# Kernel tuning notes

Measured on AMD Instinct MI355X. Metric: run time of the kernel, lower is better.

The kernel has to match this reference:

```python
import jax, jax.numpy as jnp
import numpy as np

N_NODES = 50000
N_EDGES = 1000000
HIDDEN = 64
NUM_GRAPHS = 512
EPS = 1e-5


def _instance_norm(x, seg, num_graphs):
    # per-graph, per-channel normalization (PyG InstanceNorm, affine=False)
    ones = jnp.ones((x.shape[0], 1), x.dtype)
    cnt = jnp.clip(jax.ops.segment_sum(ones, seg, num_segments=num_graphs), 1.0)
    mean = jax.ops.segment_sum(x, seg, num_segments=num_graphs) / cnt
    xc = x - mean[seg]
    var = jax.ops.segment_sum(xc * xc, seg, num_segments=num_graphs) / cnt
    return xc * jax.lax.rsqrt(var + EPS)[seg]


def setup_inputs() -> dict:
    key = jax.random.key(0)
    ks = jax.random.split(key, 10)
    emb = jax.random.normal(ks[0], (N_NODES, HIDDEN), jnp.float32)
    edge_index = jax.random.randint(ks[1], (2, N_EDGES), 0, N_NODES, jnp.int64 if jax.config.read('jax_enable_x64') else jnp.int32)
    batch = jnp.sort(jax.random.randint(ks[2], (N_NODES,), 0, NUM_GRAPHS))
    h = HIDDEN
    # channels = [2h, 4h, h, 1]
    W1 = jax.random.normal(ks[3], (2 * h, 4 * h), jnp.float32) * 0.05
    b1 = jnp.zeros((4 * h,), jnp.float32)
    W2 = jax.random.normal(ks[4], (4 * h, h), jnp.float32) * 0.05
    b2 = jnp.zeros((h,), jnp.float32)
    W3 = jax.random.normal(ks[5], (h, 1), jnp.float32) * 0.05
    b3 = jnp.zeros((1,), jnp.float32)
    return {"emb": emb, "W1": W1, "b1": b1, "W2": W2, "b2": b2,
            "W3": W3, "b3": b3, "edge_index": edge_index, "batch": batch}


def reference(emb, W1, b1, W2, b2, W3, b3, edge_index, batch):
    col, row = edge_index[0], edge_index[1]
    f12 = jnp.concatenate([emb[col], emb[row]], axis=-1)  # [E, 2h]
    seg = batch[col]  # per-edge graph id
    x = f12 @ W1 + b1                                      # [E, 4h]
    x = jax.nn.relu(_instance_norm(x, seg, NUM_GRAPHS))
    x = x @ W2 + b2                                        # [E, h]
    x = jax.nn.relu(_instance_norm(x, seg, NUM_GRAPHS))
    return x @ W3 + b3                                     # [E, 1]
```

## Files before the change

### kernel.cpp

```cpp
#include <hip/hip_runtime.h>
#include <hip/hip_bf16.h>

#define EDGES 1000000
#define NNODES 50000
#define NG 512
#define NTILES 15625
#define NCOLB 50176

typedef __attribute__((ext_vector_type(8))) short bf16x8;
typedef __attribute__((ext_vector_type(4))) float f32x4;

__device__ __forceinline__ unsigned short f2bf(float f){
  unsigned u = __float_as_uint(f);
  u += 0x7fffu + ((u >> 16) & 1u);
  return (unsigned short)(u >> 16);
}
__device__ __forceinline__ float bf2f(unsigned short h){
  return __uint_as_float(((unsigned)h) << 16);
}
__device__ __forceinline__ unsigned pk2bf(float x, float y){
  __hip_bfloat162 h = __float22bfloat162_rn(make_float2(x, y));
  union { __hip_bfloat162 h; unsigned u; } cv; cv.h = h;
  return cv.u;
}
__device__ __forceinline__ int xcd_swizzle(int bid, int nb){
  int nb8 = nb & ~7;
  if (bid >= nb8) return bid;
  int per = nb8 >> 3;
  return (bid & 7) * per + (bid >> 3);
}

__global__ void prep_all(const float* __restrict__ emb, const float* __restrict__ W1,
                         const float* __restrict__ W2,
                         unsigned short* __restrict__ emb_bf,
                         unsigned short* __restrict__ w1tn, unsigned short* __restrict__ w2t){
  int i = blockIdx.x * 256 + threadIdx.x;
  if (i < NNODES * 64){
    emb_bf[i] = f2bf(emb[i]);
  } else {
    int j = i - NNODES * 64;
    if (j < 32768){
      int jj = j >> 6, k = j & 63;
      float v = (jj < 256) ? W1[k * 256 + jj] : W1[(k + 64) * 256 + (jj - 256)];
      w1tn[j] = f2bf(v);
    } else {
      int jj = j - 32768;
      if (jj < 16384){
        int n = jj >> 8, k = jj & 255;
        w2t[jj] = f2bf(W2[k * 64 + n]);
      }
    }
  }
}

__global__ void hists(const int* __restrict__ ei, const int* __restrict__ batch,
                      unsigned* __restrict__ hist, unsigned* __restrict__ chist){
  __shared__ unsigned h[NG];
  int t = threadIdx.x;
  h[t] = 0; h[t + 256] = 0;
  __syncthreads();
  for (int i = 0; i < 4; i++){
    int e = blockIdx.x * 1024 + i * 256 + t;
    if (e < EDGES){
      int cn = ei[e];
      atomicAdd(&chist[cn], 1u);
      atomicAdd(&h[batch[cn]], 1u);
    }
  }
  __syncthreads();
  atomicAdd(&hist[t], h[t]);
  atomicAdd(&hist[t + 256], h[t + 256]);
}

__global__ void col_scan1(const unsigned* __restrict__ chist, unsigned* __restrict__ cpre,
                          unsigned* __restrict__ bsum){
  __shared__ unsigned s[256];
  int t = threadIdx.x;
  int i = blockIdx.x * 256 + t;
  unsigned v = (i < NNODES) ? chist[i] : 0u;
  s[t] = v;
  __syncthreads();
  for (int o = 1; o < 256; o <<= 1){
    unsigned u = (t >= o) ? s[t - o] : 0u;
    __syncthreads();
    s[t] += u;
    __syncthreads();
  }
  cpre[i] = s[t] - v;
  if (t == 255) bsum[blockIdx.x] = s[255];
}

__global__ void col_scan2(unsigned* __restrict__ bsum){
  __shared__ unsigned s[256];
  int t = threadIdx.x;
  unsigned v = (t < 196) ? bsum[t] : 0u;
  s[t] = v;
  __syncthreads();
  for (int o = 1; o < 256; o <<= 1){
    unsigned u = (t >= o) ? s[t - o] : 0u;
    __syncthreads();
    s[t] += u;
    __syncthreads();
  }
  if (t < 196) bsum[t] = s[t] - v;
}

__global__ void col_scan3(unsigned* __restrict__ cpre, const unsigned* __restrict__ bsum){
  int i = blockIdx.x * 256 + threadIdx.x;
  cpre[i] += bsum[blockIdx.x];
}

__global__ void col_scatter(const int* __restrict__ ei, const int* __restrict__ batch,
                            unsigned* __restrict__ cpre, int4* __restrict__ emeta){
  for (int i = 0; i < 4; i++){
    int e = blockIdx.x * 1024 + i * 256 + threadIdx.x;
    if (e < EDGES){
      int cn = ei[e];
      int pos = (int)atomicAdd(&cpre[cn], 1u);
      emeta[pos] = make_int4(cn, ei[EDGES + e], batch[cn], e);
    }
  }
}

__global__ __launch_bounds__(256) void node_gemm(
    const unsigned short* __restrict__ emb_bf, const unsigned short* __restrict__ w1tn,
    unsigned short* __restrict__ P)
{
  __shared__ unsigned short As[64 * 72];
  int t = threadIdx.x;
  int n0 = blockIdx.x * 64;
  {
    int nl = t >> 2, part = t & 3;
    int node = n0 + nl; if (node >= NNODES) node = 0;
    const int4* src = (const int4*)(emb_bf + node * 64 + part * 16);
    int4* dst = (int4*)(As + nl * 72 + part * 16);
    dst[0] = src[0]; dst[1] = src[1];
  }
  __syncthreads();
  int w = t >> 6, lane = t & 63, q = lane >> 4, c = lane & 15;
  f32x4 acc[4][8];
  for (int a = 0; a < 4; a++) for (int b = 0; b < 8; b++) for (int r = 0; r < 4; r++) acc[a][b][r] = 0.f;
  for (int k0 = 0; k0 < 64; k0 += 32){
    bf16x8 af[4];
    for (int tt = 0; tt < 4; tt++) af[tt] = *(const bf16x8*)(As + (tt * 16 + c) * 72 + k0 + q * 8);
    for (int n4 = 0; n4 < 8; n4++){
      bf16x8 bw = *(const bf16x8*)(w1tn + (w * 128 + n4 * 16 + c) * 64 + k0 + q * 8);
      for (int tt = 0; tt < 4; tt++)
        acc[tt][n4] = __builtin_amdgcn_mfma_f32_16x16x32_bf16(af[tt], bw, acc[tt][n4], 0, 0, 0);
    }
  }
  for (int tt = 0; tt < 4; tt++){
    for (int r = 0; r < 4; r++){
      int node = n0 + tt * 16 + q * 4 + r;
      if (node < NNODES){
        unsigned short* dst = P + (size_t)node * 512 + w * 128 + c;
        for (int n4 = 0; n4 < 8; n4++) dst[n4 * 16] = f2bf(acc[tt][n4][r]);
      }
    }
  }
}

__global__ __launch_bounds__(256) void k1_gather(
    const unsigned short* __restrict__ P, const int4* __restrict__ emeta,
    float* __restrict__ sum1, float* __restrict__ sqs1)
{
  int lane = threadIdx.x & 63;
  int bid = xcd_swizzle(blockIdx.x, gridDim.x);
  int wid = (bid * 256 + threadIdx.x) >> 6;
  if (wid >= NTILES) return;
  int p0 = wid * 64;
  int4 me = emeta[p0 + lane];
  int c4 = lane * 4;
  int s0 = __builtin_amdgcn_readlane(me.z, 0);
  bool uni = (__ballot(me.z == s0) == ~0ull);
  float sm0 = 0.f, sm1 = 0.f, sm2 = 0.f, sm3 = 0.f;
  float q0 = 0.f, q1 = 0.f, q2 = 0.f, q3 = 0.f;
  if (uni){
    int cprev = __builtin_amdgcn_readlane(me.x, 0);
    ushort4 a = *(const ushort4*)(P + (size_t)cprev * 512 + c4);
    ushort4 cur[4];
    #pragma unroll
    for (int j = 0; j < 4; j++){
      int re = __builtin_amdgcn_readlane(me.y, j);
      cur[j] = *(const ushort4*)(P + (size_t)re * 512 + 256 + c4);
    }
    for (int eb = 0; eb < 64; eb += 4){
      ushort4 nxt[4];
      if (eb < 60){
        #pragma unroll
        for (int j = 0; j < 4; j++){
          int re = __builtin_amdgcn_readlane(me.y, eb + 4 + j);
          nxt[j] = *(const ushort4*)(P + (size_t)re * 512 + 256 + c4);
        }
      }
      #pragma unroll
      for (int j = 0; j < 4; j++){
        int ce = __builtin_amdgcn_readlane(me.x, eb + j);
        if (ce != cprev){ a = *(const ushort4*)(P + (size_t)ce * 512 + c4); cprev = ce; }
        float x0 = bf2f(a.x) + bf2f(cur[j].x);
        float x1 = bf2f(a.y) + bf2f(cur[j].y);
        float x2v = bf2f(a.z) + bf2f(cur[j].z);
        float x3 = bf2f(a.w) + bf2f(cur[j].w);
        sm0 += x0; q0 += x0 * x0;
        sm1 += x1; q1 += x1 * x1;
        sm2 += x2v; q2 += x2v * x2v;
        sm3 += x3; q3 += x3 * x3;
      }
      #pragma unroll
      for (int j = 0; j < 4; j++) cur[j] = nxt[j];
    }
    float* sp = sum1 + s0 * 256 + c4;
    float* qp = sqs1 + s0 * 256 + c4;
    atomicAdd(sp + 0, sm0); atomicAdd(sp + 1, sm1); atomicAdd(sp + 2, sm2); atomicAdd(sp + 3, sm3);
    atomicAdd(qp + 0, q0);  atomicAdd(qp + 1, q1);  atomicAdd(qp + 2, q2);  atomicAdd(qp + 3, q3);
  } else {
    int cur = s0;
    int cprev = -1;
    ushort4 a = make_ushort4(0,0,0,0);
    for (int e = 0; e < 64; e++){
      int ce = __builtin_amdgcn_readlane(me.x, e);
      int re = __builtin_amdgcn_readlane(me.y, e);
      if (ce != cprev){ a = *(const ushort4*)(P + (size_t)ce * 512 + c4); cprev = ce; }
      ushort4 b = *(const ushort4*)(P + (size_t)re * 512 + 256 + c4);
      int s = __builtin_amdgcn_readlane(me.z, e);
      if (s != cur){
        float* sp = sum1 + cur * 256 + c4;
        float* qp = sqs1 + cur * 256 + c4;
        atomicAdd(sp + 0, sm0); atomicAdd(sp + 1, sm1); atomicAdd(sp + 2, sm2); atomicAdd(sp + 3, sm3);
        atomicAdd(qp + 0, q0);  atomicAdd(qp + 1, q1);  atomicAdd(qp + 2, q2);  atomicAdd(qp + 3, q3);
        sm0 = sm1 = sm2 = sm3 = 0.f; q0 = q1 = q2 = q3 = 0.f;
        cur = s;
      }
      float x0 = bf2f(a.x) + bf2f(b.x);
      float x1 = bf2f(a.y) + bf2f(b.y);
      float x2v = bf2f(a.z) + bf2f(b.z);
      float x3 = bf2f(a.w) + bf2f(b.w);
      sm0 += x0; q0 += x0 * x0;
      sm1 += x1; q1 += x1 * x1;
      sm2 += x2v; q2 += x2v * x2v;
      sm3 += x3; q3 += x3 * x3;
    }
    float* sp = sum1 + cur * 256 + c4;
    float* qp = sqs1 + cur * 256 + c4;
    atomicAdd(sp + 0, sm0); atomicAdd(sp + 1, sm1); atomicAdd(sp + 2, sm2); atomicAdd(sp + 3, sm3);
    atomicAdd(qp + 0, q0);  atomicAdd(qp + 1, q1);  atomicAdd(qp + 2, q2);  atomicAdd(qp + 3, q3);
  }
}

__global__ void finalize1(const float* __restrict__ sum1, const float* __restrict__ sqs1,
                          const unsigned* __restrict__ hist, float* __restrict__ r1,
                          float* __restrict__ mr1){
  int i = blockIdx.x * 256 + threadIdx.x;
  int g = i >> 8;
  float cnt = fmaxf((float)hist[g], 1.f);
  float m = sum1[i] / cnt;
  float v = sqs1[i] / cnt - m * m;
  v = fmaxf(v, 0.f);
  float r = rsqrtf(v + 1e-5f);
  r1[i] = r;
  mr1[i] = m * r;
}

__global__ void finalize2(const float* __restrict__ sum2, const float* __restrict__ sqs2,
                          const unsigned* __restrict__ hist, float* __restrict__ r2,
                          float* __restrict__ mr2){
  int i = blockIdx.x * 256 + threadIdx.x;
  int g = i >> 6;
  float cnt = fmaxf((float)hist[g], 1.f);
  float m = sum2[i] / cnt;
  float v = sqs2[i] / cnt - m * m;
  v = fmaxf(v, 0.f);
  float r = rsqrtf(v + 1e-5f);
  r2[i] = r;
  mr2[i] = m * r;
}

__global__ __launch_bounds__(256) void k2_fused(
    const unsigned short* __restrict__ P, const unsigned short* __restrict__ w2t,
    const int4* __restrict__ emeta,
    const float* __restrict__ r1, const float* __restrict__ mr1,
    float* __restrict__ sum2, float* __restrict__ sqs2,
    unsigned short* __restrict__ x2t)
{
  __shared__ unsigned short Y[64 * 264];
  __shared__ int segl[64];
  __shared__ short rsegA[64];
  __shared__ unsigned char rloA[65];
  __shared__ int nrunS;
  int t = threadIdx.x;
  int bid = xcd_swizzle(blockIdx.x, gridDim.x);
  int p0 = bid * 64;
  int w = t >> 6, lane = t & 63, q = lane >> 4, c = lane & 15;
  int c4 = lane * 4;
  int elb0 = w * 16;
  int4 me = emeta[p0 + elb0 + (lane & 15)];

  ushort4 bb[16];
  #pragma unroll
  for (int e = 0; e < 16; e++){
    int re = __builtin_amdgcn_readlane(me.y, e);
    bb[e] = *(const ushort4*)(P + (size_t)re * 512 + 256 + c4);
  }
  int cprev = __builtin_amdgcn_readlane(me.x, 0);
  ushort4 a = *(const ushort4*)(P + (size_t)cprev * 512 + c4);
  int s0g = __builtin_amdgcn_readlane(me.z, 0);
  float4 r4  = *(const float4*)(r1  + s0g * 256 + c4);
  float4 mr4 = *(const float4*)(mr1 + s0g * 256 + c4);

  if (t < 64) segl[t] = emeta[p0 + t].z;
  if (w == 0){
    int sN = segl[lane];
    int nxt = (lane < 63) ? segl[lane + 1] : sN;
    unsigned long long mask = __ballot(sN != nxt);
    if (lane == 0){
      if (mask == 0ull){
        nrunS = 1; rloA[0] = 0; rloA[1] = 64; rsegA[0] = (short)sN;
      } else {
        int n = 0, cur = segl[0];
        rsegA[0] = (short)cur; rloA[0] = 0;
        for (int i = 1; i < 64; i++)
          if (segl[i] != cur){ cur = segl[i]; n++; rsegA[n] = (short)cur; rloA[n] = (unsigned char)i; }
        rloA[n + 1] = 64; nrunS = n + 1;
      }
    }
  }
  __syncthreads();
  int nrun = nrunS;
  bool uni = (nrun == 1);

  #pragma unroll
  for (int e = 0; e < 16; e++){
    int ce = __builtin_amdgcn_readlane(me.x, e);
    if (ce != cprev){ a = *(const ushort4*)(P + (size_t)ce * 512 + c4); cprev = ce; }
    float4 rr4 = r4, mm4 = mr4;
    if (!uni){
      int s = __builtin_amdgcn_readlane(me.z, e);
      rr4 = *(const float4*)(r1  + s * 256 + c4);
      mm4 = *(const float4*)(mr1 + s * 256 + c4);
    }
    float y0 = fmaxf(0.f, (bf2f(a.x) + bf2f(bb[e].x)) * rr4.x - mm4.x);
    float y1 = fmaxf(0.f, (bf2f(a.y) + bf2f(bb[e].y)) * rr4.y - mm4.y);
    float y2 = fmaxf(0.f, (bf2f(a.z) + bf2f(bb[e].z)) * rr4.z - mm4.z);
    float y3 = fmaxf(0.f, (bf2f(a.w) + bf2f(bb[e].w)) * rr4.w - mm4.w);
    uint2 pk;
    pk.x = pk2bf(y0, y1);
    pk.y = pk2bf(y2, y3);
    *(uint2*)(Y + (elb0 + e) * 264 + c4) = pk;
  }
  __syncthreads();

  f32x4 acc2[4];
  for (int tt = 0; tt < 4; tt++) for (int r = 0; r < 4; r++) acc2[tt][r] = 0.f;
  int ch2 = w * 16 + c;
  for (int kc = 0; kc < 8; kc++){
    int k0 = kc * 32;
    bf16x8 bfr = *(const bf16x8*)(w2t + ch2 * 256 + k0 + q * 8);
    for (int tt = 0; tt < 4; tt++){
      bf16x8 afr = *(const bf16x8*)(Y + (tt * 16 + c) * 264 + k0 + q * 8);
      acc2[tt] = __builtin_amdgcn_mfma_f32_16x16x32_bf16(afr, bfr, acc2[tt], 0, 0, 0);
    }
  }

  if (uni){
    int s = segl[0];
    float sm = 0.f, sq = 0.f;
    for (int tt = 0; tt < 4; tt++)
      for (int r = 0; r < 4; r++){
        float v = acc2[tt][r];
        sm += v; sq += v * v;
      }
    sm += __shfl_xor(sm, 16); sq += __shfl_xor(sq, 16);
    sm += __shfl_xor(sm, 32); sq += __shfl_xor(sq, 32);
    if (q == 0){
      atomicAdd(&sum2[s * 64 + ch2], sm);
      atomicAdd(&sqs2[s * 64 + ch2], sq);
    }
  } else {
    for (int rr = 0; rr < nrun; rr++){
      int s = rsegA[rr], lo = rloA[rr], hi = rloA[rr + 1];
      float sm = 0.f, sq = 0.f;
      for (int tt = 0; tt < 4; tt++){
        int elb = tt * 16 + q * 4;
        for (int r = 0; r < 4; r++){
          int el = elb + r;
          if (el >= lo && el < hi){
            float v = acc2[tt][r];
            sm += v; sq += v * v;
          }
        }
      }
      sm += __shfl_xor(sm, 16); sq += __shfl_xor(sq, 16);
      sm += __shfl_xor(sm, 32); sq += __shfl_xor(sq, 32);
      if (q == 0){
        atomicAdd(&sum2[s * 64 + ch2], sm);
        atomicAdd(&sqs2[s * 64 + ch2], sq);
      }
    }
  }
  for (int tt = 0; tt < 4; tt++){
    uint2 pk;
    pk.x = pk2bf(acc2[tt][0], acc2[tt][1]);
    pk.y = pk2bf(acc2[tt][2], acc2[tt][3]);
    *(uint2*)(x2t + (size_t)ch2 * EDGES + p0 + tt * 16 + q * 4) = pk;
  }
}

__global__ __launch_bounds__(256) void k3_out(
    const unsigned short* __restrict__ x2t, const int4* __restrict__ emeta,
    const float* __restrict__ r2, const float* __restrict__ mr2,
    const float* __restrict__ W3, const float* __restrict__ b3, float* __restrict__ out)
{
  int pp4 = (blockIdx.x * 256 + threadIdx.x) * 4;
  if (pp4 >= EDGES) return;
  int4 m0 = emeta[pp4 + 0];
  int4 m1 = emeta[pp4 + 1];
  int4 m2 = emeta[pp4 + 2];
  int4 m3 = emeta[pp4 + 3];
  float a0 = 0.f, a1 = 0.f, a2 = 0.f, a3 = 0.f;
  if (m0.z == m3.z && m0.z == m1.z && m0.z == m2.z){
    const float* rp = r2  + m0.z * 64;
    const float* mp = mr2 + m0.z * 64;
    #pragma unroll 8
    for (int ch = 0; ch < 64; ch++){
      ushort4 v = *(const ushort4*)(x2t + (size_t)ch * EDGES + pp4);
      float rr = rp[ch], mm = mp[ch], wv = W3[ch];
      a0 += fmaxf(0.f, bf2f(v.x) * rr - mm) * wv;
      a1 += fmaxf(0.f, bf2f(v.y) * rr - mm) * wv;
      a2 += fmaxf(0.f, bf2f(v.z) * rr - mm) * wv;
      a3 += fmaxf(0.f, bf2f(v.w) * rr - mm) * wv;
    }
  } else {
    #pragma unroll 8
    for (int ch = 0; ch < 64; ch++){
      ushort4 v = *(const ushort4*)(x2t + (size_t)ch * EDGES + pp4);
      float wv = W3[ch];
      a0 += fmaxf(0.f, bf2f(v.x) * r2[m0.z * 64 + ch] - mr2[m0.z * 64 + ch]) * wv;
      a1 += fmaxf(0.f, bf2f(v.y) * r2[m1.z * 64 + ch] - mr2[m1.z * 64 + ch]) * wv;
      a2 += fmaxf(0.f, bf2f(v.z) * r2[m2.z * 64 + ch] - mr2[m2.z * 64 + ch]) * wv;
      a3 += fmaxf(0.f, bf2f(v.w) * r2[m3.z * 64 + ch] - mr2[m3.z * 64 + ch]) * wv;
    }
  }
  float bv = b3[0];
  out[m0.w] = a0 + bv;
  out[m1.w] = a1 + bv;
  out[m2.w] = a2 + bv;
  out[m3.w] = a3 + bv;
}

extern "C" void kernel_launch(void* const* d_in, const int* in_sizes, int n_in,
                              void* d_out, int out_size, void* d_ws, size_t ws_size,
                              hipStream_t stream)
{
  (void)in_sizes; (void)n_in; (void)out_size;
  const float* emb = (const float*)d_in[0];
  const float* W1  = (const float*)d_in[1];
  const float* W2  = (const float*)d_in[3];
  const float* W3  = (const float*)d_in[5];
  const float* b3  = (const float*)d_in[6];
  const int* ei    = (const int*)d_in[7];
  const int* batch = (const int*)d_in[8];
  float* out = (float*)d_out;

  char* p = (char*)d_ws;
  size_t off = 0;
  auto take = [&](size_t n) -> char* {
    char* r = p + off;
    off += (n + 255) & ~(size_t)255;
    return r;
  };

  unsigned short* emb_bf = (unsigned short*)take((size_t)NNODES * 64 * 2);
  unsigned short* w1tn   = (unsigned short*)take(32768 * 2);
  unsigned short* w2t    = (unsigned short*)take(16384 * 2);
  int4* emeta = (int4*)take((size_t)EDGES * 16);
  unsigned short* P   = (unsigned short*)take((size_t)NNODES * 512 * 2);
  unsigned short* x2t = (unsigned short*)take((size_t)EDGES * 64 * 2);
  float* r1  = (float*)take(512 * 256 * 4);
  float* mr1 = (float*)take(512 * 256 * 4);
  float* r2  = (float*)take(512 * 64 * 4);
  float* mr2 = (float*)take(512 * 64 * 4);
  unsigned* cpre = (unsigned*)take(NCOLB * 4);
  unsigned* bsum = (unsigned*)take(256 * 4);
  char* zbase = p + off;
  unsigned* hist  = (unsigned*)take(NG * 4);
  unsigned* chist = (unsigned*)take(NCOLB * 4);
  float* sum1 = (float*)take(512 * 256 * 4);
  float* sqs1 = (float*)take(512 * 256 * 4);
  float* sum2 = (float*)take(512 * 64 * 4);
  float* sqs2 = (float*)take(512 * 64 * 4);
  size_t zsize = (size_t)((p + off) - zbase);

  if (ws_size < off) return;

  hipMemsetAsync(zbase, 0, zsize, stream);
  prep_all<<<12692, 256, 0, stream>>>(emb, W1, W2, emb_bf, w1tn, w2t);
  hists<<<977, 256, 0, stream>>>(ei, batch, hist, chist);
  col_scan1<<<196, 256, 0, stream>>>(chist, cpre, bsum);
  col_scan2<<<1, 256, 0, stream>>>(bsum);
  col_scan3<<<196, 256, 0, stream>>>(cpre, bsum);
  col_scatter<<<977, 256, 0, stream>>>(ei, batch, cpre, emeta);
  node_gemm<<<(NNODES + 63) / 64, 256, 0, stream>>>(emb_bf, w1tn, P);
  k1_gather<<<(NTILES + 3) / 4, 256, 0, stream>>>(P, emeta, sum1, sqs1);
  finalize1<<<512, 256, 0, stream>>>(sum1, sqs1, hist, r1, mr1);
  k2_fused<<<NTILES, 256, 0, stream>>>(P, w2t, emeta, r1, mr1, sum2, sqs2, x2t);
  finalize2<<<128, 256, 0, stream>>>(sum2, sqs2, hist, r2, mr2);
  k3_out<<<977, 256, 0, stream>>>(x2t, emeta, r2, mr2, W3, b3, out);
}
```

Measured before the change: 575.6 us.

## Merge prep with histograms and node GEMM with edge scatter; convert emb inline

Weight conversion and the histogram pass now share one launch, and the node GEMM shares a launch with the column scatter, with blocks picked by index range. The GEMM reads fp32 embeddings and converts them to bf16 while staging to LDS, which removes the separate emb_bf buffer and its write/read round trip. The k2 epilogue moves into a helper that branches on nrun==1 instead of the uniform flag. This cuts two launches and the serialization between independent work, but the merged kernels run mixed block types that may compete for resources.

```diff
diff --git a/kernel.cpp b/kernel.cpp
--- a/kernel.cpp
+++ b/kernel.cpp
@@ -6,6 +6,9 @@
 #define NG 512
 #define NTILES 15625
 #define NCOLB 50176
+#define GEMMB 782
+#define HISTB 977
+#define PREPB 192
 
 typedef __attribute__((ext_vector_type(8))) short bf16x8;
 typedef __attribute__((ext_vector_type(4))) float f32x4;
@@ -30,46 +33,41 @@
   return (bid & 7) * per + (bid >> 3);
 }
 
-__global__ void prep_all(const float* __restrict__ emb, const float* __restrict__ W1,
-                         const float* __restrict__ W2,
-                         unsigned short* __restrict__ emb_bf,
-                         unsigned short* __restrict__ w1tn, unsigned short* __restrict__ w2t){
-  int i = blockIdx.x * 256 + threadIdx.x;
-  if (i < NNODES * 64){
-    emb_bf[i] = f2bf(emb[i]);
-  } else {
-    int j = i - NNODES * 64;
+__global__ void prep_hists(const float* __restrict__ W1, const float* __restrict__ W2,
+                           unsigned short* __restrict__ w1tn, unsigned short* __restrict__ w2t,
+                           const int* __restrict__ ei, const int* __restrict__ batch,
+                           unsigned* __restrict__ hist, unsigned* __restrict__ chist){
+  __shared__ unsigned h[NG];
+  if (blockIdx.x < PREPB){
+    int j = blockIdx.x * 256 + threadIdx.x;
     if (j < 32768){
       int jj = j >> 6, k = j & 63;
       float v = (jj < 256) ? W1[k * 256 + jj] : W1[(k + 64) * 256 + (jj - 256)];
       w1tn[j] = f2bf(v);
     } else {
-      int jj = j - 32768;
-      if (jj < 16384){
-        int n = jj >> 8, k = jj & 255;
-        w2t[jj] = f2bf(W2[k * 64 + n]);
-      }
-    }
-  }
-}
-
-__global__ void hists(const int* __restrict__ ei, const int* __restrict__ batch,
-                      unsigned* __restrict__ hist, unsigned* __restrict__ chist){
-  __shared__ unsigned h[NG];
-  int t = threadIdx.x;
-  h[t] = 0; h[t + 256] = 0;
-  __syncthreads();
-  for (int i = 0; i < 4; i++){
-    int e = blockIdx.x * 1024 + i * 256 + t;
-    if (e < EDGES){
-      int cn = ei[e];
-      atomicAdd(&chist[cn], 1u);
-      atomicAdd(&h[batch[cn]], 1u);
-    }
-  }
-  __syncthreads();
-  atomicAdd(&hist[t], h[t]);
-  atomicAdd(&hist[t + 256], h[t + 256]);
+      int i = j - 32768;
+      if (i < 16384){
+        int n = i >> 8, k = i & 255;
+        w2t[i] = f2bf(W2[k * 64 + n]);
+      }
+    }
+  } else {
+    int bid = blockIdx.x - PREPB;
+    int t = threadIdx.x;
+    h[t] = 0; h[t + 256] = 0;
+    __syncthreads();
+    for (int i = 0; i < 4; i++){
+      int e = bid * 1024 + i * 256 + t;
+      if (e < EDGES){
+        int cn = ei[e];
+        atomicAdd(&chist[cn], 1u);
+        atomicAdd(&h[batch[cn]], 1u);
+      }
+    }
+    __syncthreads();
+    atomicAdd(&hist[t], h[t]);
+    atomicAdd(&hist[t + 256], h[t + 256]);
+  }
 }
 
 __global__ void col_scan1(const unsigned* __restrict__ chist, unsigned* __restrict__ cpre,
@@ -110,51 +108,54 @@
   cpre[i] += bsum[blockIdx.x];
 }
 
-__global__ void col_scatter(const int* __restrict__ ei, const int* __restrict__ batch,
-                            unsigned* __restrict__ cpre, int4* __restrict__ emeta){
-  for (int i = 0; i < 4; i++){
-    int e = blockIdx.x * 1024 + i * 256 + threadIdx.x;
-    if (e < EDGES){
-      int cn = ei[e];
-      int pos = (int)atomicAdd(&cpre[cn], 1u);
-      emeta[pos] = make_int4(cn, ei[EDGES + e], batch[cn], e);
-    }
-  }
-}
-
-__global__ __launch_bounds__(256) void node_gemm(
-    const unsigned short* __restrict__ emb_bf, const unsigned short* __restrict__ w1tn,
-    unsigned short* __restrict__ P)
+__global__ __launch_bounds__(256) void gemm_scatter(
+    const float* __restrict__ emb, const unsigned short* __restrict__ w1tn,
+    unsigned short* __restrict__ P, const int* __restrict__ ei,
+    const int* __restrict__ batch, unsigned* __restrict__ cpre, int4* __restrict__ emeta)
 {
   __shared__ unsigned short As[64 * 72];
-  int t = threadIdx.x;
-  int n0 = blockIdx.x * 64;
-  {
-    int nl = t >> 2, part = t & 3;
-    int node = n0 + nl; if (node >= NNODES) node = 0;
-    const int4* src = (const int4*)(emb_bf + node * 64 + part * 16);
-    int4* dst = (int4*)(As + nl * 72 + part * 16);
-    dst[0] = src[0]; dst[1] = src[1];
-  }
-  __syncthreads();
-  int w = t >> 6, lane = t & 63, q = lane >> 4, c = lane & 15;
-  f32x4 acc[4][8];
-  for (int a = 0; a < 4; a++) for (int b = 0; b < 8; b++) for (int r = 0; r < 4; r++) acc[a][b][r] = 0.f;
-  for (int k0 = 0; k0 < 64; k0 += 32){
-    bf16x8 af[4];
-    for (int tt = 0; tt < 4; tt++) af[tt] = *(const bf16x8*)(As + (tt * 16 + c) * 72 + k0 + q * 8);
-    for (int n4 = 0; n4 < 8; n4++){
-      bf16x8 bw = *(const bf16x8*)(w1tn + (w * 128 + n4 * 16 + c) * 64 + k0 + q * 8);
-      for (int tt = 0; tt < 4; tt++)
-        acc[tt][n4] = __builtin_amdgcn_mfma_f32_16x16x32_bf16(af[tt], bw, acc[tt][n4], 0, 0, 0);
-    }
-  }
-  for (int tt = 0; tt < 4; tt++){
-    for (int r = 0; r < 4; r++){
-      int node = n0 + tt * 16 + q * 4 + r;
-      if (node < NNODES){
-        unsigned short* dst = P + (size_t)node * 512 + w * 128 + c;
-        for (int n4 = 0; n4 < 8; n4++) dst[n4 * 16] = f2bf(acc[tt][n4][r]);
+  if (blockIdx.x < GEMMB){
+    int t = threadIdx.x;
+    int n0 = blockIdx.x * 64;
+    {
+      int nl = t >> 2, part = t & 3;
+      int node = n0 + nl; if (node >= NNODES) node = 0;
+      const float4* src = (const float4*)(emb + node * 64 + part * 16);
+      float4 f0 = src[0], f1 = src[1], f2 = src[2], f3 = src[3];
+      uint4* dst = (uint4*)(As + nl * 72 + part * 16);
+      dst[0] = make_uint4(pk2bf(f0.x, f0.y), pk2bf(f0.z, f0.w), pk2bf(f1.x, f1.y), pk2bf(f1.z, f1.w));
+      dst[1] = make_uint4(pk2bf(f2.x, f2.y), pk2bf(f2.z, f2.w), pk2bf(f3.x, f3.y), pk2bf(f3.z, f3.w));
+    }
+    __syncthreads();
+    int w = t >> 6, lane = t & 63, q = lane >> 4, c = lane & 15;
+    f32x4 acc[4][8];
+    for (int a = 0; a < 4; a++) for (int b = 0; b < 8; b++) for (int r = 0; r < 4; r++) acc[a][b][r] = 0.f;
+    for (int k0 = 0; k0 < 64; k0 += 32){
+      bf16x8 af[4];
+      for (int tt = 0; tt < 4; tt++) af[tt] = *(const bf16x8*)(As + (tt * 16 + c) * 72 + k0 + q * 8);
+      for (int n4 = 0; n4 < 8; n4++){
+        bf16x8 bw = *(const bf16x8*)(w1tn + (w * 128 + n4 * 16 + c) * 64 + k0 + q * 8);
+        for (int tt = 0; tt < 4; tt++)
+          acc[tt][n4] = __builtin_amdgcn_mfma_f32_16x16x32_bf16(af[tt], bw, acc[tt][n4], 0, 0, 0);
+      }
+    }
+    for (int tt = 0; tt < 4; tt++){
+      for (int r = 0; r < 4; r++){
+        int node = n0 + tt * 16 + q * 4 + r;
+        if (node < NNODES){
+          unsigned short* dst = P + (size_t)node * 512 + w * 128 + c;
+          for (int n4 = 0; n4 < 8; n4++) dst[n4 * 16] = f2bf(acc[tt][n4][r]);
+        }
+      }
+    }
+  } else {
+    int bid = blockIdx.x - GEMMB;
+    for (int i = 0; i < 4; i++){
+      int e = bid * 1024 + i * 256 + threadIdx.x;
+      if (e < EDGES){
+        int cn = ei[e];
+        int pos = (int)atomicAdd(&cpre[cn], 1u);
+        emeta[pos] = make_int4(cn, ei[EDGES + e], batch[cn], e);
       }
     }
   }
@@ -275,6 +276,68 @@
   mr2[i] = m * r;
 }
 
+__device__ __forceinline__ void k2_tail(
+    const unsigned short* __restrict__ Y, const unsigned short* __restrict__ w2t,
+    const int* __restrict__ segl, const short* __restrict__ rsegA,
+    const unsigned char* __restrict__ rloA, int nrun,
+    float* __restrict__ sum2, float* __restrict__ sqs2, unsigned short* __restrict__ x2t,
+    int p0, int w, int q, int c)
+{
+  f32x4 acc2[4];
+  for (int tt = 0; tt < 4; tt++) for (int r = 0; r < 4; r++) acc2[tt][r] = 0.f;
+  int ch2 = w * 16 + c;
+  for (int kc = 0; kc < 8; kc++){
+    int k0 = kc * 32;
+    bf16x8 bfr = *(const bf16x8*)(w2t + ch2 * 256 + k0 + q * 8);
+    for (int tt = 0; tt < 4; tt++){
+      bf16x8 afr = *(const bf16x8*)(Y + (tt * 16 + c) * 264 + k0 + q * 8);
+      acc2[tt] = __builtin_amdgcn_mfma_f32_16x16x32_bf16(afr, bfr, acc2[tt], 0, 0, 0);
+    }
+  }
+  if (nrun == 1){
+    int s = segl[0];
+    float sm = 0.f, sq = 0.f;
+    for (int tt = 0; tt < 4; tt++)
+      for (int r = 0; r < 4; r++){
+        float v = acc2[tt][r];
+        sm += v; sq += v * v;
+      }
+    sm += __shfl_xor(sm, 16); sq += __shfl_xor(sq, 16);
+    sm += __shfl_xor(sm, 32); sq += __shfl_xor(sq, 32);
+    if (q == 0){
+      atomicAdd(&sum2[s * 64 + ch2], sm);
+      atomicAdd(&sqs2[s * 64 + ch2], sq);
+    }
+  } else {
+    for (int rr = 0; rr < nrun; rr++){
+      int s = rsegA[rr], lo = rloA[rr], hi = rloA[rr + 1];
+      float sm = 0.f, sq = 0.f;
+      for (int tt = 0; tt < 4; tt++){
+        int elb = tt * 16 + q * 4;
+        for (int r = 0; r < 4; r++){
+          int el = elb + r;
+          if (el >= lo && el < hi){
+            float v = acc2[tt][r];
+            sm += v; sq += v * v;
+          }
+        }
+      }
+      sm += __shfl_xor(sm, 16); sq += __shfl_xor(sq, 16);
+      sm += __shfl_xor(sm, 32); sq += __shfl_xor(sq, 32);
+      if (q == 0){
+        atomicAdd(&sum2[s * 64 + ch2], sm);
+        atomicAdd(&sqs2[s * 64 + ch2], sq);
+      }
+    }
+  }
+  for (int tt = 0; tt < 4; tt++){
+    uint2 pk;
+    pk.x = pk2bf(acc2[tt][0], acc2[tt][1]);
+    pk.y = pk2bf(acc2[tt][2], acc2[tt][3]);
+    *(uint2*)(x2t + (size_t)ch2 * EDGES + p0 + tt * 16 + q * 4) = pk;
+  }
+}
+
 __global__ __launch_bounds__(256) void k2_fused(
     const unsigned short* __restrict__ P, const unsigned short* __restrict__ w2t,
     const int4* __restrict__ emeta,
@@ -348,61 +411,7 @@
     *(uint2*)(Y + (elb0 + e) * 264 + c4) = pk;
   }
   __syncthreads();
-
-  f32x4 acc2[4];
-  for (int tt = 0; tt < 4; tt++) for (int r = 0; r < 4; r++) acc2[tt][r] = 0.f;
-  int ch2 = w * 16 + c;
-  for (int kc = 0; kc < 8; kc++){
-    int k0 = kc * 32;
-    bf16x8 bfr = *(const bf16x8*)(w2t + ch2 * 256 + k0 + q * 8);
-    for (int tt = 0; tt < 4; tt++){
-      bf16x8 afr = *(const bf16x8*)(Y + (tt * 16 + c) * 264 + k0 + q * 8);
-      acc2[tt] = __builtin_amdgcn_mfma_f32_16x16x32_bf16(afr, bfr, acc2[tt], 0, 0, 0);
-    }
-  }
-
-  if (uni){
-    int s = segl[0];
-    float sm = 0.f, sq = 0.f;
-    for (int tt = 0; tt < 4; tt++)
-      for (int r = 0; r < 4; r++){
-        float v = acc2[tt][r];
-        sm += v; sq += v * v;
-      }
-    sm += __shfl_xor(sm, 16); sq += __shfl_xor(sq, 16);
-    sm += __shfl_xor(sm, 32); sq += __shfl_xor(sq, 32);
-    if (q == 0){
-      atomicAdd(&sum2[s * 64 + ch2], sm);
-      atomicAdd(&sqs2[s * 64 + ch2], sq);
-    }
-  } else {
-    for (int rr = 0; rr < nrun; rr++){
-      int s = rsegA[rr], lo = rloA[rr], hi = rloA[rr + 1];
-      float sm = 0.f, sq = 0.f;
-      for (int tt = 0; tt < 4; tt++){
-        int elb = tt * 16 + q * 4;
-        for (int r = 0; r < 4; r++){
-          int el = elb + r;
-          if (el >= lo && el < hi){
-            float v = acc2[tt][r];
-            sm += v; sq += v * v;
-          }
-        }
-      }
-      sm += __shfl_xor(sm, 16); sq += __shfl_xor(sq, 16);
-      sm += __shfl_xor(sm, 32); sq += __shfl_xor(sq, 32);
-      if (q == 0){
-        atomicAdd(&sum2[s * 64 + ch2], sm);
-        atomicAdd(&sqs2[s * 64 + ch2], sq);
-      }
-    }
-  }
-  for (int tt = 0; tt < 4; tt++){
-    uint2 pk;
-    pk.x = pk2bf(acc2[tt][0], acc2[tt][1]);
-    pk.y = pk2bf(acc2[tt][2], acc2[tt][3]);
-    *(uint2*)(x2t + (size_t)ch2 * EDGES + p0 + tt * 16 + q * 4) = pk;
-  }
+  k2_tail(Y, w2t, segl, rsegA, rloA, nrun, sum2, sqs2, x2t, p0, w, q, c);
 }
 
 __global__ __launch_bounds__(256) void k3_out(
@@ -469,9 +478,8 @@
     return r;
   };
 
-  unsigned short* emb_bf = (unsigned short*)take((size_t)NNODES * 64 * 2);
-  unsigned short* w1tn   = (unsigned short*)take(32768 * 2);
-  unsigned short* w2t    = (unsigned short*)take(16384 * 2);
+  unsigned short* w1tn = (unsigned short*)take(32768 * 2);
+  unsigned short* w2t  = (unsigned short*)take(16384 * 2);
   int4* emeta = (int4*)take((size_t)EDGES * 16);
   unsigned short* P   = (unsigned short*)take((size_t)NNODES * 512 * 2);
   unsigned short* x2t = (unsigned short*)take((size_t)EDGES * 64 * 2);
@@ -493,13 +501,11 @@
   if (ws_size < off) return;
 
   hipMemsetAsync(zbase, 0, zsize, stream);
-  prep_all<<<12692, 256, 0, stream>>>(emb, W1, W2, emb_bf, w1tn, w2t);
-  hists<<<977, 256, 0, stream>>>(ei, batch, hist, chist);
+  prep_hists<<<PREPB + HISTB, 256, 0, stream>>>(W1, W2, w1tn, w2t, ei, batch, hist, chist);
   col_scan1<<<196, 256, 0, stream>>>(chist, cpre, bsum);
   col_scan2<<<1, 256, 0, stream>>>(bsum);
   col_scan3<<<196, 256, 0, stream>>>(cpre, bsum);
-  col_scatter<<<977, 256, 0, stream>>>(ei, batch, cpre, emeta);
-  node_gemm<<<(NNODES + 63) / 64, 256, 0, stream>>>(emb_bf, w1tn, P);
+  gemm_scatter<<<GEMMB + HISTB, 256, 0, stream>>>(emb, w1tn, P, ei, batch, cpre, emeta);
   k1_gather<<<(NTILES + 3) / 4, 256, 0, stream>>>(P, emeta, sum1, sqs1);
   finalize1<<<512, 256, 0, stream>>>(sum1, sqs1, hist, r1, mr1);
   k2_fused<<<NTILES, 256, 0, stream>>>(P, w2t, emeta, r1, mr1, sum2, sqs2, x2t);
```

New measurement: 587.6 us. +2.1%, slower.
